# Performance work log

Hardware: AMD Instinct MI355X
Metric: run time of the kernel (lower is better)

The kernel has to match this reference:

```python
import jax, jax.numpy as jnp
import numpy as np

D_MODEL = 768
N_HEADS = 12
D_K = D_MODEL // N_HEADS
WINDOW = 256
NEG_INF = -1e30


def setup_inputs() -> dict:
    key = jax.random.key(0)
    ks = jax.random.split(key, 9)
    s = 0.02
    x = jax.random.normal(ks[0], (2, 2048, D_MODEL), dtype=jnp.float32)
    Wq = jax.random.normal(ks[1], (D_MODEL, D_MODEL), dtype=jnp.float32) * s
    bq = jnp.zeros((D_MODEL,), dtype=jnp.float32)
    Wk = jax.random.normal(ks[2], (D_MODEL, D_MODEL), dtype=jnp.float32) * s
    bk = jnp.zeros((D_MODEL,), dtype=jnp.float32)
    Wv = jax.random.normal(ks[3], (D_MODEL, D_MODEL), dtype=jnp.float32) * s
    bv = jnp.zeros((D_MODEL,), dtype=jnp.float32)
    Wo = jax.random.normal(ks[4], (D_MODEL, D_MODEL), dtype=jnp.float32) * s
    bo = jnp.zeros((D_MODEL,), dtype=jnp.float32)
    return {"x": x, "Wq": Wq, "bq": bq, "Wk": Wk, "bk": bk,
            "Wv": Wv, "bv": bv, "Wo": Wo, "bo": bo}


def _window_mask(seq_len: int) -> jnp.ndarray:
    # Faithful to _apply_sliding_window_attention: scores are reshaped into
    # (nw, ws, nw, ws) windows and a causal tril is applied broadcast over BOTH
    # window indices => position (q, k) allowed iff (q % ws) >= (k % ws).
    # (seq_len here is a multiple of WINDOW, so pad/slice is a no-op.)
    if seq_len <= WINDOW:
        q = jnp.arange(seq_len)
        return q[:, None] >= jnp.arange(seq_len)[None, :]
    qmod = jnp.arange(seq_len) % WINDOW
    return qmod[:, None] >= qmod[None, :]


def reference(x, Wq, bq, Wk, bk, Wv, bv, Wo, bo):
    B, S, _ = x.shape
    # torch nn.Linear: y = x @ W.T + b
    q = (x @ Wq.T + bq).reshape(B, S, N_HEADS, D_K).transpose(0, 2, 1, 3)
    k = (x @ Wk.T + bk).reshape(B, S, N_HEADS, D_K).transpose(0, 2, 1, 3)
    v = (x @ Wv.T + bv).reshape(B, S, N_HEADS, D_K).transpose(0, 2, 1, 3)
    scores = jnp.einsum('bhqd,bhkd->bhqk', q, k) / jnp.sqrt(jnp.float32(D_K))
    mask = _window_mask(S)  # [S, S] bool
    scores = jnp.where(mask[None, None, :, :], scores, NEG_INF)
    probs = jax.nn.softmax(scores, axis=-1)  # dropout p=0 (eval)
    out = jnp.einsum('bhqk,bhkd->bhqd', probs, v)
    out = out.transpose(0, 2, 1, 3).reshape(B, S, D_MODEL)
    return out @ Wo.T + bo
```

## Files before the change

### kernel.cpp

```cpp
#include <hip/hip_runtime.h>

typedef unsigned short u16;
typedef unsigned int u32;
typedef unsigned long long u64;
typedef __attribute__((ext_vector_type(8))) short bfrag;
typedef __attribute__((ext_vector_type(4))) float f32x4;
typedef __attribute__((ext_vector_type(16))) float f32x16;
typedef __attribute__((ext_vector_type(4))) u32 u32x4;

#define QSCALE 0.18033688f

__device__ __forceinline__ u16 f2bf(float f) {
    unsigned u = __float_as_uint(f);
    u += 0x7FFFu + ((u >> 16) & 1u);
    return (u16)(u >> 16);
}

__device__ __forceinline__ u32 cvt_pk_bf16(float lo, float hi) {
    u32 r;
    asm("v_cvt_pk_bf16_f32 %0, %1, %2" : "=v"(r) : "v"(lo), "v"(hi));
    return r;
}

__device__ __forceinline__ void glds16(const void* g, void* l) {
    __builtin_amdgcn_global_load_lds((__attribute__((address_space(1))) void*)g,
                                     (__attribute__((address_space(3))) void*)l,
                                     16, 0, 0);
}

__device__ __forceinline__ f32x16 mfma32(bfrag a, bfrag b, f32x16 c) {
    return __builtin_amdgcn_mfma_f32_32x32x16_bf16(a, b, c, 0, 0, 0);
}

#define WAIT_VM4()  asm volatile("s_waitcnt vmcnt(4)" ::: "memory")
#define WAIT_VM3()  asm volatile("s_waitcnt vmcnt(3)" ::: "memory")
#define WAIT_VM0()  asm volatile("s_waitcnt vmcnt(0)" ::: "memory")
#define BAR()       __builtin_amdgcn_s_barrier()
#define SCHED_FENCE() __builtin_amdgcn_sched_barrier(0)
#define PRIO(n)     __builtin_amdgcn_s_setprio(n)

__global__ __launch_bounds__(256) void convert_all(
    const float* __restrict__ x, const float* __restrict__ wq,
    const float* __restrict__ wk, const float* __restrict__ wv,
    const float* __restrict__ wo,
    u16* __restrict__ xb, u16* __restrict__ wqb, u16* __restrict__ wkb,
    u16* __restrict__ wvb, u16* __restrict__ wob) {
    const int XV = (2 * 2048 * 768) / 4;
    const int WV = (768 * 768) / 4;
    int i = blockIdx.x * 256 + threadIdx.x;
    if (i >= XV + 4 * WV) return;
    const float4* src; u16* dst; int off;
    if (i < XV) { src = (const float4*)x; dst = xb; off = i; }
    else {
        int j = i - XV; int z = j / WV; off = j - z * WV;
        src = (const float4*)(z == 0 ? wq : z == 1 ? wk : z == 2 ? wv : wo);
        dst = (z == 0 ? wqb : z == 1 ? wkb : z == 2 ? wvb : wob);
    }
    float4 v = src[off];
    u64 pk = (u64)f2bf(v.x)
        | ((u64)f2bf(v.y) << 16)
        | ((u64)f2bf(v.z) << 32)
        | ((u64)f2bf(v.w) << 48);
    *(u64*)(dst + off * 4) = pk;
}

__device__ __forceinline__ void gemm_core64(
    const u16* __restrict__ A, const u16* __restrict__ Bw, int m0,
    u16* a_lds, u16* b_lds, f32x4 acc[2][4]) {
    const int t = threadIdx.x;
    const int w = t >> 6, lane = t & 63, ln = lane & 15, lh = lane >> 4;
    const int wr = w >> 1, wc = w & 1;

    const int rowA = t >> 2;
    const int uA = (t & 3) ^ ((rowA >> 1) & 3);
    const int rowB1 = rowA + 64;
    const int uB1 = (t & 3) ^ ((rowB1 >> 1) & 3);
    const u16* ga  = A + (m0 + rowA) * 768 + uA * 8;
    const u16* gb0 = Bw + rowA * 768 + uA * 8;
    const u16* gb1 = Bw + rowB1 * 768 + uB1 * 8;
    u16* la = a_lds + w * 512;
    u16* lb = b_lds + w * 512;

    auto STAGE = [&](int k0, int bi) {
        glds16(ga + k0, la + bi * 2048);
        glds16(gb0 + k0, lb + bi * 4096);
        glds16(gb1 + k0, lb + bi * 4096 + 2048);
    };

    STAGE(0, 0);
    int cur = 0;
    for (int k0 = 0; k0 < 768; k0 += 32) {
        if (k0 + 32 < 768) {
            STAGE(k0 + 32, cur ^ 1);
            WAIT_VM3();
        } else {
            WAIT_VM0();
        }
        BAR();
        SCHED_FENCE();
        const u16* ab = a_lds + cur * 2048;
        const u16* bb = b_lds + cur * 4096;
        bfrag aF[2], bF[4];
#pragma unroll
        for (int i = 0; i < 2; i++) {
            int ra = wr * 32 + i * 16 + ln;
            aF[i] = *(const bfrag*)(ab + ra * 32 + ((lh ^ ((ra >> 1) & 3)) * 8));
        }
#pragma unroll
        for (int j = 0; j < 4; j++) {
            int rb = wc * 64 + j * 16 + ln;
            bF[j] = *(const bfrag*)(bb + rb * 32 + ((lh ^ ((rb >> 1) & 3)) * 8));
        }
#pragma unroll
        for (int i = 0; i < 2; i++)
#pragma unroll
            for (int j = 0; j < 4; j++)
                acc[i][j] = __builtin_amdgcn_mfma_f32_16x16x32_bf16(
                    aF[i], bF[j], acc[i][j], 0, 0, 0);
        SCHED_FENCE();
        BAR();
        cur ^= 1;
    }
}

__global__ __launch_bounds__(256) void gemm_qkv64(
    const u16* __restrict__ xb,
    const u16* __restrict__ wqb, const u16* __restrict__ wkb, const u16* __restrict__ wvb,
    const float* __restrict__ bq, const float* __restrict__ bk, const float* __restrict__ bv,
    u16* __restrict__ q_ws, u16* __restrict__ k_ws, u16* __restrict__ vt_ws) {
    __shared__ __align__(16) u16 smem[12288];
    u16* a_lds = smem;
    u16* b_lds = smem + 4096;
    const int m0 = blockIdx.x * 64;
    const int z = blockIdx.y / 6, nb = blockIdx.y % 6;
    const u16* Bw = (z == 0 ? wqb : z == 1 ? wkb : wvb) + nb * 128 * 768;
    const float* bias = (z == 0 ? bq : z == 1 ? bk : bv);

    f32x4 acc[2][4] = {};
    gemm_core64(xb, Bw, m0, a_lds, b_lds, acc);

    const int t = threadIdx.x, w = t >> 6, lane = t & 63, ln = lane & 15, lh = lane >> 4;
    const int wr = w >> 1, wc = w & 1;
    if (z == 2) {
        __syncthreads();
        char* T = (char*)smem;
#pragma unroll
        for (int j = 0; j < 4; j++) {
            int nt = wc * 64 + j * 16 + ln;
            float bb = bias[nb * 128 + nt];
#pragma unroll
            for (int i = 0; i < 2; i++) {
                int m0t = wr * 32 + i * 16 + lh * 4;
                u64 pk = (u64)f2bf(acc[i][j][0] + bb)
                    | ((u64)f2bf(acc[i][j][1] + bb) << 16)
                    | ((u64)f2bf(acc[i][j][2] + bb) << 32)
                    | ((u64)f2bf(acc[i][j][3] + bb) << 48);
                int off = nt * 128 + ((((m0t >> 3) ^ (nt & 7)) << 4)) + ((m0t & 7) * 2);
                *(u64*)(T + off) = pk;
            }
        }
        __syncthreads();
        const int b = m0 >> 11, s0 = m0 & 2047;
#pragma unroll
        for (int c = 0; c < 4; c++) {
            int g = c * 256 + t;
            int nt = g >> 3, mu = g & 7;
            int off = nt * 128 + ((mu ^ (nt & 7)) << 4);
            u32x4 v = *(const u32x4*)(T + off);
            int nl = nb * 128 + nt;
            int h = nl >> 6, d = nl & 63;
            *(u32x4*)(vt_ws + ((size_t)((b * 12 + h) * 64 + d)) * 2048 + s0 + mu * 8) = v;
        }
    } else {
        u16* dst = (z == 0 ? q_ws : k_ws);
        const float sc = (z == 0) ? QSCALE : 1.0f;
#pragma unroll
        for (int j = 0; j < 4; j++) {
            int nl = nb * 128 + wc * 64 + j * 16 + ln;
            int h = nl >> 6, d = nl & 63;
            float bb = bias[nl];
#pragma unroll
            for (int i = 0; i < 2; i++)
#pragma unroll
                for (int r = 0; r < 4; r++) {
                    int m = m0 + wr * 32 + i * 16 + lh * 4 + r;
                    int b = m >> 11, s = m & 2047;
                    dst[((size_t)((b * 12 + h) * 2048 + s)) * 64 + d] = f2bf((acc[i][j][r] + bb) * sc);
                }
        }
    }
}

__global__ __launch_bounds__(256) void gemm_out64(
    const u16* __restrict__ ob, const u16* __restrict__ wob,
    const float* __restrict__ bo, float* __restrict__ out) {
    __shared__ __align__(16) u16 a_lds[2 * 64 * 32];
    __shared__ __align__(16) u16 b_lds[2 * 128 * 32];
    const int m0 = blockIdx.x * 64, n0 = blockIdx.y * 128;
    f32x4 acc[2][4] = {};
    gemm_core64(ob, wob + n0 * 768, m0, a_lds, b_lds, acc);
    const int t = threadIdx.x, w = t >> 6, lane = t & 63, ln = lane & 15, lh = lane >> 4;
    const int wr = w >> 1, wc = w & 1;
#pragma unroll
    for (int j = 0; j < 4; j++) {
        int n = n0 + wc * 64 + j * 16 + ln;
        float bb = bo[n];
#pragma unroll
        for (int i = 0; i < 2; i++)
#pragma unroll
            for (int r = 0; r < 4; r++) {
                int m = m0 + wr * 32 + i * 16 + lh * 4 + r;
                out[m * 768 + n] = acc[i][j][r] + bb;
            }
    }
}

__global__ __launch_bounds__(256) void attn8(
    const u16* __restrict__ q_ws, const u16* __restrict__ k_ws,
    const u16* __restrict__ vt_ws, u16* __restrict__ o_ws,
    u16* __restrict__ po_ws, float* __restrict__ l_ws) {
    __shared__ __align__(16) u16 k_lds[2][64 * 64];
    __shared__ __align__(16) u16 v_lds[2][64 * 64];

    const int t = threadIdx.x, w = t >> 6, l = t & 63, lq = l & 31, H = l >> 5;
    int id = blockIdx.x;
    int bh8 = id & 7, idq = id >> 3;
    int bhq = idq % 3, pg = idq / 3;
    int t7, rem;
    if (pg < 16)      { t7 = 7 - (pg >> 3); rem = pg & 7; }
    else if (pg < 28) { int u = pg - 16; t7 = 5 - u / 6; rem = u % 6; }
    else if (pg < 36) { int u = pg - 28; t7 = 3 - (u >> 2); rem = u & 3; }
    else              { int u = pg - 36; t7 = 1 - (u >> 1); rem = u & 1; }
    const int np = (t7 + 2) >> 1;
    const int quad = rem / np, piece = rem - quad * np;
    const int bh = bhq * 8 + bh8;
    const int ti = quad * 4 + w;
    const int tile = t7 + 8 * ti;
    const int qw0 = tile * 32;

    const u16* Qb = q_ws + (size_t)bh * 2048 * 64;
    const u16* Kb = k_ws + (size_t)bh * 2048 * 64;
    const u16* Vt = vt_ws + (size_t)bh * 64 * 2048;

    const int lqp = (lq & 19) | ((lq & 4) << 1) | ((lq & 8) >> 1);
    const int ksw = lqp & 7;
    const int vsw = lq & 7;

    bfrag qF[4];
#pragma unroll
    for (int kd = 0; kd < 4; kd++)
        qF[kd] = *(const bfrag*)(Qb + (size_t)(qw0 + lq) * 64 + kd * 16 + H * 8);

    const f32x16 Z = {};
    f32x16 O0 = Z, O1 = Z;
    float lsum = 0.f;

    const int skey = t >> 3;
    const int su = (t & 7) ^ (skey & 7);

    auto STAGE = [&](int k0, int bi) {
        glds16(Kb + (size_t)(k0 + skey) * 64 + su * 8,        k_lds[bi] + w * 512);
        glds16(Kb + (size_t)(k0 + skey + 32) * 64 + su * 8,   k_lds[bi] + 2048 + w * 512);
        glds16(Vt + (size_t)skey * 2048 + k0 + su * 8,        v_lds[bi] + w * 512);
        glds16(Vt + (size_t)(skey + 32) * 2048 + k0 + su * 8, v_lds[bi] + 2048 + w * 512);
    };

    int gp0 = piece * 8;
    int win = gp0 / np, pb = gp0 - win * np;
    STAGE(win * 256 + pb * 64, 0);

    for (int j = 0; j < 8; ++j) {
        int winn = win, pbn = pb + 1;
        if (pbn == np) { pbn = 0; winn = win + 1; }
        if (j < 7) {
            STAGE(winn * 256 + pbn * 64, (j + 1) & 1);
            WAIT_VM4();
        } else {
            WAIT_VM0();
        }
        BAR();
        SCHED_FENCE();

        const int cb = 2 * pb;
        const bool c1 = (cb + 1) <= t7, d0 = (cb == t7), d1 = (cb + 1 == t7);
        const u16* kl = k_lds[j & 1];
        const u16* vl = v_lds[j & 1];

        PRIO(1);
        f32x16 s0, s1;
        {
            bfrag kf = *(const bfrag*)(kl + lqp * 64 + ((H) ^ ksw) * 8);
            s0 = mfma32(kf, qF[0], Z);
#pragma unroll
            for (int kd = 1; kd < 4; kd++) {
                bfrag k2 = *(const bfrag*)(kl + lqp * 64 + ((kd * 2 + H) ^ ksw) * 8);
                s0 = mfma32(k2, qF[kd], s0);
            }
        }
        if (c1) {
            bfrag kf = *(const bfrag*)(kl + (32 + lqp) * 64 + ((H) ^ ksw) * 8);
            s1 = mfma32(kf, qF[0], Z);
#pragma unroll
            for (int kd = 1; kd < 4; kd++) {
                bfrag k2 = *(const bfrag*)(kl + (32 + lqp) * 64 + ((kd * 2 + H) ^ ksw) * 8);
                s1 = mfma32(k2, qF[kd], s1);
            }
        }
        PRIO(0);

        float ps = 0.f;
        u32 pkA[8], pkB[8];
        if (d0) {
#pragma unroll
            for (int r2 = 0; r2 < 16; r2++) {
                int ka = (r2 & 3) + 4 * ((r2 >> 2) & 1) + 16 * (r2 >> 3) + 8 * H;
                if (ka > lq) s0[r2] = -1e30f;
            }
        }
#pragma unroll
        for (int i = 0; i < 8; i++) {
            float a = exp2f(s0[2 * i]), b2 = exp2f(s0[2 * i + 1]);
            ps += a + b2; pkA[i] = cvt_pk_bf16(a, b2);
        }
        if (c1) {
            if (d1) {
#pragma unroll
                for (int r2 = 0; r2 < 16; r2++) {
                    int ka = (r2 & 3) + 4 * ((r2 >> 2) & 1) + 16 * (r2 >> 3) + 8 * H;
                    if (ka > lq) s1[r2] = -1e30f;
                }
            }
#pragma unroll
            for (int i = 0; i < 8; i++) {
                float a = exp2f(s1[2 * i]), b2 = exp2f(s1[2 * i + 1]);
                ps += a + b2; pkB[i] = cvt_pk_bf16(a, b2);
            }
        }
        lsum += ps;

        PRIO(1);
        {
            u32x4 a0 = {pkA[0], pkA[1], pkA[2], pkA[3]};
            u32x4 a1 = {pkA[4], pkA[5], pkA[6], pkA[7]};
            bfrag A0 = __builtin_bit_cast(bfrag, a0);
            bfrag A1 = __builtin_bit_cast(bfrag, a1);
            bfrag v00 = *(const bfrag*)(vl + lq * 64 + ((H) ^ vsw) * 8);
            bfrag v01 = *(const bfrag*)(vl + (32 + lq) * 64 + ((H) ^ vsw) * 8);
            bfrag v10 = *(const bfrag*)(vl + lq * 64 + ((2 + H) ^ vsw) * 8);
            bfrag v11 = *(const bfrag*)(vl + (32 + lq) * 64 + ((2 + H) ^ vsw) * 8);
            O0 = mfma32(A0, v00, O0);
            O1 = mfma32(A0, v01, O1);
            O0 = mfma32(A1, v10, O0);
            O1 = mfma32(A1, v11, O1);
        }
        if (c1) {
            u32x4 a0 = {pkB[0], pkB[1], pkB[2], pkB[3]};
            u32x4 a1 = {pkB[4], pkB[5], pkB[6], pkB[7]};
            bfrag A0 = __builtin_bit_cast(bfrag, a0);
            bfrag A1 = __builtin_bit_cast(bfrag, a1);
            bfrag v00 = *(const bfrag*)(vl + lq * 64 + ((4 + H) ^ vsw) * 8);
            bfrag v01 = *(const bfrag*)(vl + (32 + lq) * 64 + ((4 + H) ^ vsw) * 8);
            bfrag v10 = *(const bfrag*)(vl + lq * 64 + ((6 + H) ^ vsw) * 8);
            bfrag v11 = *(const bfrag*)(vl + (32 + lq) * 64 + ((6 + H) ^ vsw) * 8);
            O0 = mfma32(A0, v00, O0);
            O1 = mfma32(A0, v01, O1);
            O0 = mfma32(A1, v10, O0);
            O1 = mfma32(A1, v11, O1);
        }
        PRIO(0);
        SCHED_FENCE();
        BAR();
        win = winn; pb = pbn;
    }

    float lsT = lsum + __shfl_xor(lsum, 32);
    if (np == 1) {
        float linv = 1.f / lsT;
        const int b = bh / 12, h = bh % 12;
#pragma unroll
        for (int r2 = 0; r2 < 16; r2++) {
            int row = (r2 & 3) + 8 * (r2 >> 2) + 4 * H;
            float fr = __shfl(linv, row);
            size_t base = ((size_t)(b * 2048 + qw0 + row)) * 768 + h * 64;
            o_ws[base + lq] = f2bf(O0[r2] * fr);
            o_ws[base + 32 + lq] = f2bf(O1[r2] * fr);
        }
    } else {
        const int cum8[8] = {0, 8, 16, 32, 48, 72, 96, 128};
        size_t pidx = (size_t)bh * 160 + cum8[t7] + ti * np + piece;
        u16* po = po_ws + pidx * 2048;
#pragma unroll
        for (int r2 = 0; r2 < 16; r2++) {
            int row = (r2 & 3) + 8 * (r2 >> 2) + 4 * H;
            po[row * 64 + lq] = f2bf(O0[r2]);
            po[row * 64 + 32 + lq] = f2bf(O1[r2]);
        }
        if (l < 32) l_ws[pidx * 32 + lq] = lsT;
    }
}

__global__ __launch_bounds__(256) void combine_o(
    const u16* __restrict__ po_ws, const float* __restrict__ l_ws,
    u16* __restrict__ o_ws) {
    int id = blockIdx.x;
    int bh8 = id & 7, idq = id >> 3;
    int bhq = idq % 3, r = idq / 3;
    int bh = bhq * 8 + bh8;
    int t7 = 2 + (r >> 3), ti = r & 7;
    int tile = t7 + 8 * ti;
    int np = (t7 + 2) >> 1;
    const int cum8[8] = {0, 8, 16, 32, 48, 72, 96, 128};
    size_t base = (size_t)bh * 160 + cum8[t7] + ti * np;
    int t = threadIdx.x;
    int q = t >> 3, d8 = (t & 7) * 8;
    float acc[8] = {0.f, 0.f, 0.f, 0.f, 0.f, 0.f, 0.f, 0.f};
    float lt = 0.f;
    for (int i = 0; i < np; i++) {
        lt += l_ws[(base + i) * 32 + q];
        bfrag v = *(const bfrag*)(po_ws + (base + i) * 2048 + q * 64 + d8);
#pragma unroll
        for (int e = 0; e < 8; e++)
            acc[e] += __uint_as_float(((u32)(u16)v[e]) << 16);
    }
    float inv = 1.f / lt;
    u32x4 pkv;
#pragma unroll
    for (int e = 0; e < 4; e++)
        pkv[e] = cvt_pk_bf16(acc[2 * e] * inv, acc[2 * e + 1] * inv);
    int b = bh / 12, h = bh % 12;
    size_t dst = ((size_t)(b * 2048 + tile * 32 + q)) * 768 + h * 64 + d8;
    *(u32x4*)(o_ws + dst) = pkv;
}

extern "C" void kernel_launch(void* const* d_in, const int* in_sizes, int n_in,
                              void* d_out, int out_size, void* d_ws, size_t ws_size,
                              hipStream_t stream) {
    const float* x  = (const float*)d_in[0];
    const float* Wq = (const float*)d_in[1];
    const float* bq = (const float*)d_in[2];
    const float* Wk = (const float*)d_in[3];
    const float* bk = (const float*)d_in[4];
    const float* Wv = (const float*)d_in[5];
    const float* bv = (const float*)d_in[6];
    const float* Wo = (const float*)d_in[7];
    const float* bo = (const float*)d_in[8];
    float* out = (float*)d_out;

    char* p = (char*)d_ws;
    u16*   q_ws  = (u16*)(p + 0);
    u16*   k_ws  = (u16*)(p + 6291456);
    u16*   vt_ws = (u16*)(p + 12582912);
    u16*   po_ws = (u16*)(p + 18874368);
    u16*   xb    = (u16*)(p + 18874368);
    u16*   wqb   = (u16*)(p + 25165824);
    u16*   wkb   = (u16*)(p + 26345472);
    u16*   wvb   = (u16*)(p + 27525120);
    float* l_ws  = (float*)(p + 34603008);
    u16*   wob   = (u16*)(p + 35094528);
    u16*   o_ws  = (u16*)(p + 36274176);

    convert_all<<<5376, 256, 0, stream>>>(x, Wq, Wk, Wv, Wo, xb, wqb, wkb, wvb, wob);
    gemm_qkv64<<<dim3(64, 18), 256, 0, stream>>>(xb, wqb, wkb, wvb, bq, bk, bv, q_ws, k_ws, vt_ws);
    attn8<<<dim3(960), 256, 0, stream>>>(q_ws, k_ws, vt_ws, o_ws, po_ws, l_ws);
    combine_o<<<dim3(1152), 256, 0, stream>>>(po_ws, l_ws, o_ws);
    gemm_out64<<<dim3(64, 6), 256, 0, stream>>>(o_ws, wob, bo, out);
}
```

Baseline: 91.48 us.

## Widen QKV projection GEMM tile to 64x256 with one head per wave

Replaces the 64x128 QKV GEMM with a 64x256 tile kernel where each wave computes a full 64-column head slice (4x4 MFMA 16x16 tiles). This halves the grid to 576 blocks, doubles A-tile reuse per block, and lets the V-transpose epilogue write per-head contiguous output. It costs more LDS and accumulator registers per block and leaves fewer blocks to fill the 256 CUs, which may reduce occupancy and load balance.

```diff
diff --git a/kernel.cpp b/kernel.cpp
--- a/kernel.cpp
+++ b/kernel.cpp
@@ -32,6 +32,7 @@
     return __builtin_amdgcn_mfma_f32_32x32x16_bf16(a, b, c, 0, 0, 0);
 }
 
+#define WAIT_VM5()  asm volatile("s_waitcnt vmcnt(5)" ::: "memory")
 #define WAIT_VM4()  asm volatile("s_waitcnt vmcnt(4)" ::: "memory")
 #define WAIT_VM3()  asm volatile("s_waitcnt vmcnt(3)" ::: "memory")
 #define WAIT_VM0()  asm volatile("s_waitcnt vmcnt(0)" ::: "memory")
@@ -64,6 +65,120 @@
     *(u64*)(dst + off * 4) = pk;
 }
 
+__global__ __launch_bounds__(256) void gemm_qkv256(
+    const u16* __restrict__ xb,
+    const u16* __restrict__ wqb, const u16* __restrict__ wkb, const u16* __restrict__ wvb,
+    const float* __restrict__ bq, const float* __restrict__ bk, const float* __restrict__ bv,
+    u16* __restrict__ q_ws, u16* __restrict__ k_ws, u16* __restrict__ vt_ws) {
+    __shared__ __align__(16) u16 smem[20480];
+    u16* a_lds = smem;
+    u16* b_lds = smem + 4096;
+    const int m0 = blockIdx.x * 64;
+    const int z = blockIdx.y / 3, nb = blockIdx.y % 3;
+    const u16* Bw = (z == 0 ? wqb : z == 1 ? wkb : wvb) + nb * 256 * 768;
+    const float* bias = (z == 0 ? bq : z == 1 ? bk : bv);
+
+    const int t = threadIdx.x, w = t >> 6, lane = t & 63, ln = lane & 15, lh = lane >> 4;
+
+    const int rowS = t >> 2;
+    const int uS = (t & 3) ^ ((rowS >> 1) & 3);
+    const u16* ga = xb + (m0 + rowS) * 768 + uS * 8;
+    const u16* gb0 = Bw + (rowS) * 768 + uS * 8;
+    const u16* gb1 = Bw + (64 + rowS) * 768 + uS * 8;
+    const u16* gb2 = Bw + (128 + rowS) * 768 + uS * 8;
+    const u16* gb3 = Bw + (192 + rowS) * 768 + uS * 8;
+
+    auto STAGE = [&](int k0, int bi) {
+        glds16(ga + k0, a_lds + bi * 2048 + w * 512);
+        glds16(gb0 + k0, b_lds + bi * 8192 + w * 512);
+        glds16(gb1 + k0, b_lds + bi * 8192 + 2048 + w * 512);
+        glds16(gb2 + k0, b_lds + bi * 8192 + 4096 + w * 512);
+        glds16(gb3 + k0, b_lds + bi * 8192 + 6144 + w * 512);
+    };
+
+    f32x4 acc[4][4] = {};
+    STAGE(0, 0);
+    int cur = 0;
+    for (int k0 = 0; k0 < 768; k0 += 32) {
+        if (k0 + 32 < 768) {
+            STAGE(k0 + 32, cur ^ 1);
+            WAIT_VM5();
+        } else {
+            WAIT_VM0();
+        }
+        BAR();
+        SCHED_FENCE();
+        const u16* ab = a_lds + cur * 2048;
+        const u16* bb = b_lds + cur * 8192;
+        bfrag aF[4], bF[4];
+#pragma unroll
+        for (int i = 0; i < 4; i++) {
+            int ra = i * 16 + ln;
+            aF[i] = *(const bfrag*)(ab + ra * 32 + ((lh ^ ((ra >> 1) & 3)) * 8));
+            int rb = w * 64 + i * 16 + ln;
+            bF[i] = *(const bfrag*)(bb + rb * 32 + ((lh ^ ((rb >> 1) & 3)) * 8));
+        }
+#pragma unroll
+        for (int i = 0; i < 4; i++)
+#pragma unroll
+            for (int j = 0; j < 4; j++)
+                acc[i][j] = __builtin_amdgcn_mfma_f32_16x16x32_bf16(
+                    aF[i], bF[j], acc[i][j], 0, 0, 0);
+        SCHED_FENCE();
+        BAR();
+        cur ^= 1;
+    }
+
+    if (z == 2) {
+        __syncthreads();
+        char* T = (char*)smem;
+#pragma unroll
+        for (int j = 0; j < 4; j++) {
+            int dt = j * 16 + ln;
+            float bbias = bias[nb * 256 + w * 64 + dt];
+#pragma unroll
+            for (int i = 0; i < 4; i++) {
+                int m0t = i * 16 + lh * 4;
+                u64 pk = (u64)f2bf(acc[i][j][0] + bbias)
+                    | ((u64)f2bf(acc[i][j][1] + bbias) << 16)
+                    | ((u64)f2bf(acc[i][j][2] + bbias) << 32)
+                    | ((u64)f2bf(acc[i][j][3] + bbias) << 48);
+                int off = w * 8192 + dt * 128 + ((((m0t >> 3) ^ (dt & 7)) << 4)) + (m0t & 7) * 2;
+                *(u64*)(T + off) = pk;
+            }
+        }
+        __syncthreads();
+        const int b = m0 >> 11, s0 = m0 & 2047;
+        const int h = nb * 4 + w;
+        const int l6 = t & 63;
+#pragma unroll
+        for (int c = 0; c < 8; c++) {
+            int g = c * 64 + l6;
+            int dt = g >> 3, mu = g & 7;
+            int off = w * 8192 + dt * 128 + ((mu ^ (dt & 7)) << 4);
+            u32x4 v = *(const u32x4*)(T + off);
+            *(u32x4*)(vt_ws + ((size_t)((b * 12 + h) * 64 + dt)) * 2048 + s0 + mu * 8) = v;
+        }
+    } else {
+        u16* dst = (z == 0 ? q_ws : k_ws);
+        const float sc = (z == 0) ? QSCALE : 1.0f;
+#pragma unroll
+        for (int j = 0; j < 4; j++) {
+            int zcol = nb * 256 + w * 64 + j * 16 + ln;
+            int h = zcol >> 6, d = zcol & 63;
+            float bbias = bias[zcol];
+#pragma unroll
+            for (int i = 0; i < 4; i++)
+#pragma unroll
+                for (int r = 0; r < 4; r++) {
+                    int m = m0 + i * 16 + lh * 4 + r;
+                    int b = m >> 11, s = m & 2047;
+                    dst[((size_t)((b * 12 + h) * 2048 + s)) * 64 + d] = f2bf((acc[i][j][r] + bbias) * sc);
+                }
+        }
+    }
+}
+
 __device__ __forceinline__ void gemm_core64(
     const u16* __restrict__ A, const u16* __restrict__ Bw, int m0,
     u16* a_lds, u16* b_lds, f32x4 acc[2][4]) {
@@ -120,74 +235,6 @@
         SCHED_FENCE();
         BAR();
         cur ^= 1;
-    }
-}
-
-__global__ __launch_bounds__(256) void gemm_qkv64(
-    const u16* __restrict__ xb,
-    const u16* __restrict__ wqb, const u16* __restrict__ wkb, const u16* __restrict__ wvb,
-    const float* __restrict__ bq, const float* __restrict__ bk, const float* __restrict__ bv,
-    u16* __restrict__ q_ws, u16* __restrict__ k_ws, u16* __restrict__ vt_ws) {
-    __shared__ __align__(16) u16 smem[12288];
-    u16* a_lds = smem;
-    u16* b_lds = smem + 4096;
-    const int m0 = blockIdx.x * 64;
-    const int z = blockIdx.y / 6, nb = blockIdx.y % 6;
-    const u16* Bw = (z == 0 ? wqb : z == 1 ? wkb : wvb) + nb * 128 * 768;
-    const float* bias = (z == 0 ? bq : z == 1 ? bk : bv);
-
-    f32x4 acc[2][4] = {};
-    gemm_core64(xb, Bw, m0, a_lds, b_lds, acc);
-
-    const int t = threadIdx.x, w = t >> 6, lane = t & 63, ln = lane & 15, lh = lane >> 4;
-    const int wr = w >> 1, wc = w & 1;
-    if (z == 2) {
-        __syncthreads();
-        char* T = (char*)smem;
-#pragma unroll
-        for (int j = 0; j < 4; j++) {
-            int nt = wc * 64 + j * 16 + ln;
-            float bb = bias[nb * 128 + nt];
-#pragma unroll
-            for (int i = 0; i < 2; i++) {
-                int m0t = wr * 32 + i * 16 + lh * 4;
-                u64 pk = (u64)f2bf(acc[i][j][0] + bb)
-                    | ((u64)f2bf(acc[i][j][1] + bb) << 16)
-                    | ((u64)f2bf(acc[i][j][2] + bb) << 32)
-                    | ((u64)f2bf(acc[i][j][3] + bb) << 48);
-                int off = nt * 128 + ((((m0t >> 3) ^ (nt & 7)) << 4)) + ((m0t & 7) * 2);
-                *(u64*)(T + off) = pk;
-            }
-        }
-        __syncthreads();
-        const int b = m0 >> 11, s0 = m0 & 2047;
-#pragma unroll
-        for (int c = 0; c < 4; c++) {
-            int g = c * 256 + t;
-            int nt = g >> 3, mu = g & 7;
-            int off = nt * 128 + ((mu ^ (nt & 7)) << 4);
-            u32x4 v = *(const u32x4*)(T + off);
-            int nl = nb * 128 + nt;
-            int h = nl >> 6, d = nl & 63;
-            *(u32x4*)(vt_ws + ((size_t)((b * 12 + h) * 64 + d)) * 2048 + s0 + mu * 8) = v;
-        }
-    } else {
-        u16* dst = (z == 0 ? q_ws : k_ws);
-        const float sc = (z == 0) ? QSCALE : 1.0f;
-#pragma unroll
-        for (int j = 0; j < 4; j++) {
-            int nl = nb * 128 + wc * 64 + j * 16 + ln;
-            int h = nl >> 6, d = nl & 63;
-            float bb = bias[nl];
-#pragma unroll
-            for (int i = 0; i < 2; i++)
-#pragma unroll
-                for (int r = 0; r < 4; r++) {
-                    int m = m0 + wr * 32 + i * 16 + lh * 4 + r;
-                    int b = m >> 11, s = m & 2047;
-                    dst[((size_t)((b * 12 + h) * 2048 + s)) * 64 + d] = f2bf((acc[i][j][r] + bb) * sc);
-                }
-        }
     }
 }
 
@@ -460,7 +507,7 @@
     u16*   o_ws  = (u16*)(p + 36274176);
 
     convert_all<<<5376, 256, 0, stream>>>(x, Wq, Wk, Wv, Wo, xb, wqb, wkb, wvb, wob);
-    gemm_qkv64<<<dim3(64, 18), 256, 0, stream>>>(xb, wqb, wkb, wvb, bq, bk, bv, q_ws, k_ws, vt_ws);
+    gemm_qkv256<<<dim3(64, 9), 256, 0, stream>>>(xb, wqb, wkb, wvb, bq, bk, bv, q_ws, k_ws, vt_ws);
     attn8<<<dim3(960), 256, 0, stream>>>(q_ws, k_ws, vt_ws, o_ws, po_ws, l_ws);
     combine_o<<<dim3(1152), 256, 0, stream>>>(po_ws, l_ws, o_ws);
     gemm_out64<<<dim3(64, 6), 256, 0, stream>>>(o_ws, wob, bo, out);
```

After: 94.04 us. 1.03x slower.
